# Optimization experiments

Measured on AMD Instinct MI355X. Metric: run time of the kernel, lower is better.

The kernel has to match this reference:

```python
import jax, jax.numpy as jnp
import numpy as np

DIM = 512
HEADS = 8
DIM_HEAD = 64
INNER = HEADS * DIM_HEAD
SCALE = DIM_HEAD ** -0.5


def setup_inputs() -> dict:
    key = jax.random.key(0)
    ks = jax.random.split(key, 6)
    x = jax.random.normal(ks[0], (8, 1024, DIM), dtype=jnp.float32)
    # nn.Linear(dim, inner, bias=False): y = x @ W.T ; store W as [out, in]
    wq = jax.random.normal(ks[1], (INNER, DIM), dtype=jnp.float32) * (DIM ** -0.5)
    wk = jax.random.normal(ks[2], (INNER, DIM), dtype=jnp.float32) * (DIM ** -0.5)
    wv = jax.random.normal(ks[3], (INNER, DIM), dtype=jnp.float32) * (DIM ** -0.5)
    wo = jax.random.normal(ks[4], (DIM, INNER), dtype=jnp.float32) * (INNER ** -0.5)
    bo = jax.random.normal(ks[5], (DIM,), dtype=jnp.float32) * 0.01
    return {"x": x, "wq": wq, "wk": wk, "wv": wv, "wo": wo, "bo": bo}


def reference(x, wq, wk, wv, wo, bo):
    b, n, _ = x.shape
    # QKV projections -> [b, h, n, d]
    def proj(w):
        return (x @ w.T).reshape(b, n, HEADS, DIM_HEAD).transpose(0, 2, 1, 3)
    q, k, v = proj(wq), proj(wk), proj(wv)
    dots = jnp.einsum('bhid,bhjd->bhij', q, k) * SCALE
    dots = jnp.clip(dots, 1e-6, 1.0)
    dots_exp = jnp.exp(dots)
    attn = dots_exp / jnp.sum(dots_exp, axis=-1, keepdims=True)
    out = jnp.einsum('bhij,bhjd->bhid', attn, v)  # [b,h,n,d]
    out = out.transpose(0, 2, 1, 3).reshape(b, n, INNER)
    return out @ wo.T + bo
```

## Files before the change

kernel.cpp:

```cpp
#include <hip/hip_runtime.h>
#include <hip/hip_fp16.h>

#define BATCH 8
#define SEQ   1024
#define DIM   512
#define HEADS 8
#define DHEAD 64
#define MTOT  (BATCH*SEQ)

typedef _Float16 f16x8 __attribute__((ext_vector_type(8)));
typedef _Float16 f16x4 __attribute__((ext_vector_type(4)));
typedef float    fx4   __attribute__((ext_vector_type(4)));

#define MFMA16 __builtin_amdgcn_mfma_f32_16x16x32_f16

__device__ __forceinline__ void gload16(const _Float16* g, _Float16* l) {
    __builtin_amdgcn_global_load_lds(
        (const __attribute__((address_space(1))) unsigned int*)g,
        (__attribute__((address_space(3))) unsigned int*)l, 16, 0, 0);
}

__global__ __launch_bounds__(256) void convert_k(
    const float* __restrict__ x,  const float* __restrict__ wq,
    const float* __restrict__ wk, const float* __restrict__ wv,
    const float* __restrict__ wo,
    _Float16* __restrict__ xb, _Float16* __restrict__ wqkvb,
    _Float16* __restrict__ wob)
{
    const int XU = (MTOT*DIM)/4;
    const int WU = (DIM*DIM)/4;
    int idx = blockIdx.x*256 + threadIdx.x;
    if (idx >= XU + 4*WU) return;
    const float* src; _Float16* dst;
    if (idx < XU) { src = x + idx*4; dst = xb + idx*4; }
    else {
        int t = idx - XU; int region = t >> 16; int off = (t & 65535)*4;
        if      (region == 0) { src = wq + off; dst = wqkvb + off; }
        else if (region == 1) { src = wk + off; dst = wqkvb + DIM*DIM + off; }
        else if (region == 2) { src = wv + off; dst = wqkvb + 2*DIM*DIM + off; }
        else                  { src = wo + off; dst = wob + off; }
    }
    float4 v = *(const float4*)src;
    f16x4 o = { (_Float16)v.x, (_Float16)v.y, (_Float16)v.z, (_Float16)v.w };
    *(f16x4*)dst = o;
}

__global__ __launch_bounds__(256,3) void qkv_proj(
    const _Float16* __restrict__ X, const _Float16* __restrict__ W,
    _Float16* __restrict__ Qb, _Float16* __restrict__ Kb,
    _Float16* __restrict__ VTb)
{
    __shared__ _Float16 lA[128*64];
    __shared__ _Float16 lB[128*64];
    const int tid = threadIdx.x;
    const int w = tid>>6, l = tid&63, lr = l&15, lq = l>>4;
    const int wr = w>>1, wc = w&1;
    const int srow = (l>>3);
    const int scol = ((l&7) ^ srow)*8;
    const int sw = lr&7;
    const bool qk = blockIdx.x < 8;
    const _Float16 *pA, *pB;
    int m0, n0;
    if (qk) { m0 = blockIdx.x*128; n0 = blockIdx.y*128;
              pA = W + (size_t)m0*DIM; pB = X + (size_t)n0*DIM; }
    else    { m0 = blockIdx.y*128; n0 = 1024 + (blockIdx.x-8)*128;
              pA = X + (size_t)m0*DIM; pB = W + (size_t)n0*DIM; }
    fx4 acc[4][4] = {};

    for (int k0 = 0; k0 < DIM; k0 += 64) {
        __syncthreads();
#pragma unroll
        for (int t = 0; t < 4; t++) {
            int row = w*32 + t*8;
            gload16(&pA[(size_t)(row+srow)*DIM + k0 + scol], &lA[row*64]);
            gload16(&pB[(size_t)(row+srow)*DIM + k0 + scol], &lB[row*64]);
        }
        __syncthreads();
#pragma unroll
        for (int kb = 0; kb < 2; kb++) {
            f16x8 af[4], bf[4];
#pragma unroll
            for (int cb = 0; cb < 4; cb++)
                bf[cb] = *(const f16x8*)&lB[(wc*64+cb*16+lr)*64 + (((kb*4+lq)^sw))*8];
#pragma unroll
            for (int rb = 0; rb < 4; rb++)
                af[rb] = *(const f16x8*)&lA[(wr*64+rb*16+lr)*64 + (((kb*4+lq)^sw))*8];
#pragma unroll
            for (int rb = 0; rb < 4; rb++)
#pragma unroll
                for (int cb = 0; cb < 4; cb++)
                    acc[rb][cb] = MFMA16(af[rb], bf[cb], acc[rb][cb], 0,0,0);
        }
    }
    if (qk) {
#pragma unroll
        for (int rb = 0; rb < 4; rb++)
#pragma unroll
            for (int cb = 0; cb < 4; cb++) {
                int od = m0 + wr*64 + rb*16 + lq*4;
                int sq = n0 + wc*64 + cb*16 + lr;
                int b = sq >> 10, n = sq & 1023;
                int which = od >> 9, h = (od >> 6) & 7, d0 = od & 63;
                f16x4 v4;
                if (which == 0) {
#pragma unroll
                    for (int i = 0; i < 4; i++) v4[i] = (_Float16)(acc[rb][cb][i]*0.125f);
                    *(f16x4*)&Qb[((size_t)(b*HEADS+h)*SEQ + n)*DHEAD + d0] = v4;
                } else {
#pragma unroll
                    for (int i = 0; i < 4; i++) v4[i] = (_Float16)acc[rb][cb][i];
                    *(f16x4*)&Kb[((size_t)(b*HEADS+h)*SEQ + n)*DHEAD + d0] = v4;
                }
            }
    } else {
#pragma unroll
        for (int rb = 0; rb < 4; rb++)
#pragma unroll
            for (int cb = 0; cb < 4; cb++) {
                int inner = (n0 - 1024) + wc*64 + cb*16 + lr;
                int h = inner >> 6, d = inner & 63;
                int m = m0 + wr*64 + rb*16 + lq*4;
                int b = m >> 10, n = m & 1023;
                f16x4 v4;
#pragma unroll
                for (int i = 0; i < 4; i++) v4[i] = (_Float16)acc[rb][cb][i];
                *(f16x4*)&VTb[((size_t)(b*HEADS+h)*DHEAD + d)*SEQ + n] = v4;
            }
    }
}

__global__ __launch_bounds__(256,3) void attn_k(
    const _Float16* __restrict__ Q, const _Float16* __restrict__ K,
    const _Float16* __restrict__ VT, _Float16* __restrict__ AO)
{
    __shared__ __align__(16) char smem[53248];
    _Float16* lK  = (_Float16*)smem;
    _Float16* lVT = (_Float16*)(smem + 16384);
    _Float16* lPT = (_Float16*)(smem + 32768);
    _Float16* oscr = (_Float16*)smem;
    float* lsumBuf = (float*)(smem + 32768);

    const int tid = threadIdx.x;
    const int w = tid>>6, l = tid&63, lr = l&15, lq = l>>4;
    const int sw = lr&7;
    const int bh = blockIdx.y, q0 = blockIdx.x*64;
    const int b = bh>>3, h = bh&7;
    const _Float16* Qp = Q  + (size_t)bh*SEQ*DHEAD;
    const _Float16* Kp = K  + (size_t)bh*SEQ*DHEAD;
    const _Float16* Vp = VT + (size_t)bh*DHEAD*SEQ;
    _Float16* lPw = lPT + w*2560;

    const int kst_r = (l>>3), kst_c = ((l&7) ^ ((l>>3)&7))*8;
    const int vst_r = (l>>4);

    f16x8 qf[4][2];
#pragma unroll
    for (int qg = 0; qg < 4; qg++)
#pragma unroll
        for (int kb = 0; kb < 2; kb++)
            qf[qg][kb] = *(const f16x8*)&Qp[(q0+qg*16+lr)*DHEAD + kb*32 + lq*8];

    fx4 O[4][4] = {};
    float lsum[4] = {};

    for (int kt = 0; kt < 8; kt++) {
        int k0 = kt*128;
        __syncthreads();
#pragma unroll
        for (int t = 0; t < 4; t++) {
            int rbase = w*32 + t*8;
            gload16(&Kp[(size_t)(k0+rbase+kst_r)*DHEAD + kst_c], &lK[rbase*64]);
        }
#pragma unroll
        for (int t = 0; t < 4; t++) {
            int rbase = w*16 + t*4;
            int r = rbase + vst_r;
            int g = (l&15) ^ (r&7);
            gload16(&Vp[(size_t)r*SEQ + k0 + g*8], &lVT[rbase*128]);
        }
        __syncthreads();

#pragma unroll
        for (int rb2 = 0; rb2 < 2; rb2++) {
            int jrow = w*32 + rb2*16 + lr;
            f16x8 kf0 = *(const f16x8*)&lK[jrow*64 + ((lq^sw))*8];
            f16x8 kf1 = *(const f16x8*)&lK[jrow*64 + (((4+lq)^sw))*8];
#pragma unroll
            for (int qg = 0; qg < 4; qg++) {
                fx4 s = {};
                s = MFMA16(kf0, qf[qg][0], s, 0,0,0);
                s = MFMA16(kf1, qf[qg][1], s, 0,0,0);
                f16x4 p4;
#pragma unroll
                for (int i = 0; i < 4; i++) {
                    float p = __expf(__builtin_amdgcn_fmed3f(s[i], 1e-6f, 1.0f));
                    lsum[qg] += p;
                    p4[i] = (_Float16)p;
                }
                *(f16x4*)&lPw[(qg*16+lr)*40 + rb2*16 + lq*4] = p4;
            }
        }
        f16x8 vf[4];
#pragma unroll
        for (int db = 0; db < 4; db++)
            vf[db] = *(const f16x8*)&lVT[(db*16+lr)*128 + (((w*4+lq)^sw))*8];
#pragma unroll
        for (int qg = 0; qg < 4; qg++) {
            f16x8 pf = *(const f16x8*)&lPw[(qg*16+lr)*40 + lq*8];
#pragma unroll
            for (int db = 0; db < 4; db++)
                O[db][qg] = MFMA16(vf[db], pf, O[db][qg], 0,0,0);
        }
    }

#pragma unroll
    for (int qg = 0; qg < 4; qg++) {
        lsum[qg] += __shfl_xor(lsum[qg], 16);
        lsum[qg] += __shfl_xor(lsum[qg], 32);
    }
    __syncthreads();
    if (lq == 0) {
#pragma unroll
        for (int qg = 0; qg < 4; qg++)
            lsumBuf[w*64 + qg*16 + lr] = lsum[qg];
    }
    if (w > 0) {
        _Float16* oo = oscr + (w-1)*4352;
#pragma unroll
        for (int db = 0; db < 4; db++)
#pragma unroll
            for (int qg = 0; qg < 4; qg++) {
                f16x4 t;
#pragma unroll
                for (int i = 0; i < 4; i++) t[i] = (_Float16)O[db][qg][i];
                *(f16x4*)&oo[(qg*16+lr)*68 + db*16 + lq*4] = t;
            }
    }
    __syncthreads();
    if (w == 0) {
#pragma unroll
        for (int qg = 0; qg < 4; qg++) {
            float tot = lsum[qg] + lsumBuf[64 + qg*16+lr]
                      + lsumBuf[128 + qg*16+lr] + lsumBuf[192 + qg*16+lr];
            float inv = 1.0f / tot;
            int q = q0 + qg*16 + lr;
            _Float16* aop = AO + ((size_t)(b*SEQ + q)*HEADS + h)*DHEAD;
#pragma unroll
            for (int db = 0; db < 4; db++) {
                fx4 o = O[db][qg];
#pragma unroll
                for (int ww = 1; ww < 4; ww++) {
                    f16x4 t = *(const f16x4*)
                        &oscr[(ww-1)*4352 + (qg*16+lr)*68 + db*16 + lq*4];
#pragma unroll
                    for (int i = 0; i < 4; i++) o[i] += (float)t[i];
                }
                f16x4 r;
#pragma unroll
                for (int i = 0; i < 4; i++) r[i] = (_Float16)(o[i] * inv);
                *(f16x4*)&aop[db*16 + lq*4] = r;
            }
        }
    }
}

__global__ __launch_bounds__(256,3) void out_proj(
    const _Float16* __restrict__ Wo, const _Float16* __restrict__ Ain,
    const float* __restrict__ bo, float* __restrict__ out)
{
    __shared__ _Float16 lA[128*64];
    __shared__ _Float16 lB[128*64];
    const int tid = threadIdx.x;
    const int m0 = blockIdx.x*128, n0 = blockIdx.y*128;
    const int w = tid>>6, l = tid&63, lr = l&15, lq = l>>4;
    const int wr = w>>1, wc = w&1;
    const int srow = (l>>3);
    const int scol = ((l&7) ^ srow)*8;
    const int sw = lr&7;
    const _Float16* pA = Wo + (size_t)m0*DIM;
    const _Float16* pB = Ain + (size_t)n0*DIM;
    fx4 acc[4][4] = {};

    for (int k0 = 0; k0 < DIM; k0 += 64) {
        __syncthreads();
#pragma unroll
        for (int t = 0; t < 4; t++) {
            int row = w*32 + t*8;
            gload16(&pA[(size_t)(row+srow)*DIM + k0 + scol], &lA[row*64]);
            gload16(&pB[(size_t)(row+srow)*DIM + k0 + scol], &lB[row*64]);
        }
        __syncthreads();
#pragma unroll
        for (int kb = 0; kb < 2; kb++) {
            f16x8 af[4], bf[4];
#pragma unroll
            for (int cb = 0; cb < 4; cb++)
                bf[cb] = *(const f16x8*)&lB[(wc*64+cb*16+lr)*64 + (((kb*4+lq)^sw))*8];
#pragma unroll
            for (int rb = 0; rb < 4; rb++)
                af[rb] = *(const f16x8*)&lA[(wr*64+rb*16+lr)*64 + (((kb*4+lq)^sw))*8];
#pragma unroll
            for (int rb = 0; rb < 4; rb++)
#pragma unroll
                for (int cb = 0; cb < 4; cb++)
                    acc[rb][cb] = MFMA16(af[rb], bf[cb], acc[rb][cb], 0,0,0);
        }
    }
#pragma unroll
    for (int rb = 0; rb < 4; rb++)
#pragma unroll
        for (int cb = 0; cb < 4; cb++) {
            int od = m0 + wr*64 + rb*16 + lq*4;
            int sq = n0 + wc*64 + cb*16 + lr;
            float4 bias = *(const float4*)&bo[od];
            float4 r;
            r.x = acc[rb][cb][0] + bias.x;
            r.y = acc[rb][cb][1] + bias.y;
            r.z = acc[rb][cb][2] + bias.z;
            r.w = acc[rb][cb][3] + bias.w;
            *(float4*)&out[(size_t)sq*DIM + od] = r;
        }
}

extern "C" void kernel_launch(void* const* d_in, const int* in_sizes, int n_in,
                              void* d_out, int out_size, void* d_ws, size_t ws_size,
                              hipStream_t stream)
{
    const float* x  = (const float*)d_in[0];
    const float* wq = (const float*)d_in[1];
    const float* wk = (const float*)d_in[2];
    const float* wv = (const float*)d_in[3];
    const float* wo = (const float*)d_in[4];
    const float* bo = (const float*)d_in[5];
    float* out = (float*)d_out;
    char* ws = (char*)d_ws;

    _Float16* xb    = (_Float16*)(ws);
    _Float16* wqkvb = (_Float16*)(ws + 8388608);
    _Float16* wob   = (_Float16*)(ws + 9961472);
    _Float16* Qb    = (_Float16*)(ws + 10485760);
    _Float16* Kb    = (_Float16*)(ws + 18874368);
    _Float16* VTb   = (_Float16*)(ws + 27262976);
    _Float16* attnb = (_Float16*)(ws);

    convert_k<<<5120, 256, 0, stream>>>(x, wq, wk, wv, wo, xb, wqkvb, wob);
    qkv_proj<<<dim3(12, 64), 256, 0, stream>>>(xb, wqkvb, Qb, Kb, VTb);
    attn_k<<<dim3(16, 64), 256, 0, stream>>>(Qb, Kb, VTb, attnb);
    out_proj<<<dim3(4, 64), 256, 0, stream>>>(wob, attnb, bo, out);
}
```

Before: 154.7 us.

## Keep softmax probabilities in registers using 16x16x16 MFMA, shrink K/V tiles

Each wave now computes scores for a 16-key slice and feeds the fp16 probabilities straight from the S accumulator layout into a 16x16x16 MFMA for P·V. This removes the LDS round-trip for P and the LDS it needed. Key tiles shrink from 128 to 64 rows, which halves the K/V LDS footprint but doubles the number of loop iterations and barriers. The K=16 MFMA has lower throughput per instruction than the K=32 variant it replaces.

After: 148.3 us. -4.1%, faster.

```diff
diff --git a/kernel.cpp b/kernel.cpp
--- a/kernel.cpp
+++ b/kernel.cpp
@@ -13,6 +13,7 @@
 typedef float    fx4   __attribute__((ext_vector_type(4)));
 
 #define MFMA16 __builtin_amdgcn_mfma_f32_16x16x32_f16
+#define MFMA16K16 __builtin_amdgcn_mfma_f32_16x16x16f16
 
 __device__ __forceinline__ void gload16(const _Float16* g, _Float16* l) {
     __builtin_amdgcn_global_load_lds(
@@ -133,12 +134,11 @@
     const _Float16* __restrict__ Q, const _Float16* __restrict__ K,
     const _Float16* __restrict__ VT, _Float16* __restrict__ AO)
 {
-    __shared__ __align__(16) char smem[53248];
+    __shared__ __align__(16) char smem[27648];
     _Float16* lK  = (_Float16*)smem;
-    _Float16* lVT = (_Float16*)(smem + 16384);
-    _Float16* lPT = (_Float16*)(smem + 32768);
+    _Float16* lVT = (_Float16*)(smem + 8192);
     _Float16* oscr = (_Float16*)smem;
-    float* lsumBuf = (float*)(smem + 32768);
+    float* lsumBuf = (float*)(smem + 26112);
 
     const int tid = threadIdx.x;
     const int w = tid>>6, l = tid&63, lr = l&15, lq = l>>4;
@@ -148,10 +148,9 @@
     const _Float16* Qp = Q  + (size_t)bh*SEQ*DHEAD;
     const _Float16* Kp = K  + (size_t)bh*SEQ*DHEAD;
     const _Float16* Vp = VT + (size_t)bh*DHEAD*SEQ;
-    _Float16* lPw = lPT + w*2560;
-
-    const int kst_r = (l>>3), kst_c = ((l&7) ^ ((l>>3)&7))*8;
-    const int vst_r = (l>>4);
+
+    const int st_r = (l>>3);
+    const int st_c = ((l&7) ^ (st_r&7))*8;
 
     f16x8 qf[4][2];
 #pragma unroll
@@ -163,53 +162,45 @@
     fx4 O[4][4] = {};
     float lsum[4] = {};
 
-    for (int kt = 0; kt < 8; kt++) {
-        int k0 = kt*128;
-        __syncthreads();
-#pragma unroll
-        for (int t = 0; t < 4; t++) {
-            int rbase = w*32 + t*8;
-            gload16(&Kp[(size_t)(k0+rbase+kst_r)*DHEAD + kst_c], &lK[rbase*64]);
-        }
-#pragma unroll
-        for (int t = 0; t < 4; t++) {
-            int rbase = w*16 + t*4;
-            int r = rbase + vst_r;
-            int g = (l&15) ^ (r&7);
-            gload16(&Vp[(size_t)r*SEQ + k0 + g*8], &lVT[rbase*128]);
-        }
-        __syncthreads();
-
-#pragma unroll
-        for (int rb2 = 0; rb2 < 2; rb2++) {
-            int jrow = w*32 + rb2*16 + lr;
-            f16x8 kf0 = *(const f16x8*)&lK[jrow*64 + ((lq^sw))*8];
-            f16x8 kf1 = *(const f16x8*)&lK[jrow*64 + (((4+lq)^sw))*8];
-#pragma unroll
-            for (int qg = 0; qg < 4; qg++) {
-                fx4 s = {};
-                s = MFMA16(kf0, qf[qg][0], s, 0,0,0);
-                s = MFMA16(kf1, qf[qg][1], s, 0,0,0);
-                f16x4 p4;
-#pragma unroll
-                for (int i = 0; i < 4; i++) {
-                    float p = __expf(__builtin_amdgcn_fmed3f(s[i], 1e-6f, 1.0f));
-                    lsum[qg] += p;
-                    p4[i] = (_Float16)p;
-                }
-                *(f16x4*)&lPw[(qg*16+lr)*40 + rb2*16 + lq*4] = p4;
-            }
-        }
-        f16x8 vf[4];
-#pragma unroll
-        for (int db = 0; db < 4; db++)
-            vf[db] = *(const f16x8*)&lVT[(db*16+lr)*128 + (((w*4+lq)^sw))*8];
+    for (int kt = 0; kt < 16; kt++) {
+        int k0 = kt*64;
+        __syncthreads();
+#pragma unroll
+        for (int t = 0; t < 2; t++) {
+            int rbase = w*16 + t*8;
+            int r = rbase + st_r;
+            gload16(&Kp[(size_t)(k0+r)*DHEAD + st_c], &lK[rbase*64]);
+        }
+#pragma unroll
+        for (int t = 0; t < 2; t++) {
+            int rbase = w*16 + t*8;
+            int r = rbase + st_r;
+            gload16(&Vp[(size_t)r*SEQ + k0 + st_c], &lVT[rbase*64]);
+        }
+        __syncthreads();
+
+        f16x8 kf0 = *(const f16x8*)&lK[(w*16+lr)*64 + ((lq^sw))*8];
+        f16x8 kf1 = *(const f16x8*)&lK[(w*16+lr)*64 + (((4+lq)^sw))*8];
+        f16x4 p4[4];
 #pragma unroll
         for (int qg = 0; qg < 4; qg++) {
-            f16x8 pf = *(const f16x8*)&lPw[(qg*16+lr)*40 + lq*8];
-#pragma unroll
-            for (int db = 0; db < 4; db++)
-                O[db][qg] = MFMA16(vf[db], pf, O[db][qg], 0,0,0);
+            fx4 s = {};
+            s = MFMA16(kf0, qf[qg][0], s, 0,0,0);
+            s = MFMA16(kf1, qf[qg][1], s, 0,0,0);
+#pragma unroll
+            for (int i = 0; i < 4; i++) {
+                float p = __expf(__builtin_amdgcn_fmed3f(s[i], 1e-6f, 1.0f));
+                lsum[qg] += p;
+                p4[qg][i] = (_Float16)p;
+            }
+        }
+#pragma unroll
+        for (int db = 0; db < 4; db++) {
+            f16x4 vf = *(const f16x4*)
+                &lVT[(db*16+lr)*64 + (((w*2+(lq>>1)) ^ sw)<<3) + (lq&1)*4];
+#pragma unroll
+            for (int qg = 0; qg < 4; qg++)
+                O[db][qg] = MFMA16K16(vf, p4[qg], O[db][qg], 0,0,0);
         }
     }
 
```
